# Kernel tuning notes

Measured on AMD Instinct MI355X. Metric: run time of the kernel, lower is better.

The kernel has to match this reference:

```python
import jax, jax.numpy as jnp
import numpy as np

B, L, DM = 2, 1024, 768
DI = 2 * DM            # d_inner = 1536
NS = 16                # d_state
DTR = 48               # dt_rank
SCALE = 15             # scale_bits


def _dsp(x):
    # DampenedSquareplus: 0.5 * squareplus(x) = 0.25*(x + sqrt(x^2+4))
    return 0.25 * (x + jnp.sqrt(x * x + 4.0))


def _forward(hidden_states, gamma, W_in, b_in, conv_w, conv_b, W_x, b_x,
             W_dt, b_dt, W_out, b_out, base_decay_nums, res_gate, decay_shifts):
    residual = hidden_states
    # BitShiftNorm: center, then power-of-two RMS scale
    xm = hidden_states - hidden_states.mean(axis=-1, keepdims=True)
    var = (xm * xm).mean(axis=-1, keepdims=True)
    k = jnp.maximum(jnp.round(jnp.log2(jnp.sqrt(var + 1e-9))), 0.0)
    hs = xm * (2.0 ** (-k)) * gamma
    # in_proj (BitLinear modeled as linear)
    xz = hs @ W_in.T + b_in                      # [B,L,2*DI]
    x, z = jnp.split(xz, 2, axis=-1)             # each [B,L,DI]
    # causal depthwise conv1d (kernel 4, left pad 3, truncate to L)
    xt = jnp.transpose(x, (0, 2, 1))             # [B,DI,L]
    xt = jax.lax.conv_general_dilated(
        xt, conv_w, window_strides=(1,), padding=[(3, 0)],
        dimension_numbers=('NCH', 'OIH', 'NCH'), feature_group_count=DI)
    xt = xt + conv_b[None, :, None]
    x = jnp.transpose(xt, (0, 2, 1))             # [B,L,DI]
    x = _dsp(x)
    # x_proj -> dt, B_ssm, C_ssm
    x_dbl = x @ W_x.T + b_x                      # [B,L,DTR+2*NS]
    dt = x_dbl[..., :DTR]
    B_ssm = x_dbl[..., DTR:DTR + NS]
    C_ssm = x_dbl[..., DTR + NS:]
    decay_mod = dt @ W_dt.T + b_dt               # [B,L,DI]
    decay_nums = jnp.clip(base_decay_nums[None, None] + decay_mod[..., None], 0.0, 32767.0)  # [B,L,DI,NS]
    dt_val = _dsp(decay_mod) * 0.1               # [B,L,DI]
    u = (x * dt_val)[..., None] * B_ssm[:, :, None, :]   # [B,L,DI,NS]
    # dyadic decay: a = nums * 2^{-shift}
    a = decay_nums * (2.0 ** (-decay_shifts.astype(jnp.float32)))[None, None]
    F = DI * NS
    u_f = u.reshape(B, L, F)
    a_f = a.reshape(B, L, F)
    # linear recurrence h_t = a_t*h_{t-1} + u_t via associative scan over L
    def combine(c1, c2):
        a1, b1 = c1
        a2, b2 = c2
        return (a1 * a2, a2 * b1 + b2)
    _, h_f = jax.lax.associative_scan(combine, (a_f, u_f), axis=1)
    h_f = jnp.clip(h_f, -32000.0, 32000.0)
    h = h_f.reshape(B, L, DI, NS)
    y = jnp.einsum('bldn,bln->bld', h, C_ssm)    # [B,L,DI]
    # RationalSigmoid gate
    gate = 0.5 * (1.0 + z / jnp.sqrt(z * z + 1.0))
    y = y * gate
    out = y @ W_out.T + b_out
    out = jnp.clip(out, -32000.0, 32000.0)
    return residual + out * res_gate


def setup_inputs() -> dict:
    key = jax.random.key(0)
    ks = jax.random.split(key, 8)
    hidden_states = jax.random.normal(ks[0], (B, L, DM), jnp.float32)
    gamma = jnp.ones((DM,), jnp.float32)
    W_in = jax.random.normal(ks[1], (2 * DI, DM), jnp.float32) / np.float32(np.sqrt(DM))
    b_in = jnp.zeros((2 * DI,), jnp.float32)
    conv_w = jax.random.normal(ks[2], (DI, 1, 4), jnp.float32) * 0.5
    conv_b = jnp.zeros((DI,), jnp.float32)
    W_x = jax.random.normal(ks[3], (DTR + 2 * NS, DI), jnp.float32) / np.float32(np.sqrt(DI))
    b_x = jnp.zeros((DTR + 2 * NS,), jnp.float32)
    W_dt = jax.random.normal(ks[4], (DI, DTR), jnp.float32) * 0.001
    b_dt = jnp.zeros((DI,), jnp.float32)
    W_out = jax.random.normal(ks[5], (DM, DI), jnp.float32) * np.float32(0.02 / np.sqrt(24))
    b_out = jnp.zeros((DM,), jnp.float32)
    # HiPPO-S4D-real-like decays projected to dyadic with shift=15
    n = jnp.arange(NS, dtype=jnp.float32)
    decays = jnp.exp(-0.01 * (n + 1.0))
    base = jnp.round(decays * (2.0 ** SCALE))
    base_decay_nums = jnp.tile(base[None, :], (DI, 1))
    decay_shifts = jnp.full((DI, NS), SCALE, jnp.int32)
    res_gate = jnp.full((1,), 0.5, jnp.float32)  # nonzero so output depends on branch
    return dict(hidden_states=hidden_states, gamma=gamma, W_in=W_in, b_in=b_in,
                conv_w=conv_w, conv_b=conv_b, W_x=W_x, b_x=b_x, W_dt=W_dt, b_dt=b_dt,
                W_out=W_out, b_out=b_out, base_decay_nums=base_decay_nums,
                res_gate=res_gate, decay_shifts=decay_shifts)


def reference(hidden_states, gamma, W_in, b_in, conv_w, conv_b, W_x, b_x,
              W_dt, b_dt, W_out, b_out, base_decay_nums, res_gate, decay_shifts):
    return _forward(hidden_states, gamma, W_in, b_in, conv_w, conv_b, W_x, b_x,
                    W_dt, b_dt, W_out, b_out, base_decay_nums, res_gate, decay_shifts)
```

## Files before the change

kernel.cpp:

```cpp
#include <hip/hip_runtime.h>
#include <hip/hip_bf16.h>
#include <stdint.h>

#define BB  2
#define LL  1024
#define DMM 768
#define DII 1536
#define NSS 16
#define DTRR 48
#define XZN (2*DII)
#define NROWS (BB*LL)
#define N2 1664

#define CHUNKS 64
#define CHLEN  (LL/CHUNKS)
#define NCH    (BB*DII*NSS)

typedef _Float16 h16;
typedef __attribute__((ext_vector_type(8))) _Float16 h16x8;
typedef __attribute__((ext_vector_type(4))) float f32x4;

typedef const __attribute__((address_space(1))) uint32_t gau32;
typedef __attribute__((address_space(3))) uint32_t lau32;
#define GLL16(gp, lp) __builtin_amdgcn_global_load_lds((gau32*)(gp), (lau32*)(lp), 16, 0, 0)

__device__ __forceinline__ float dspf(float x) {
    return 0.25f * (x + sqrtf(x*x + 4.0f));
}
__device__ __forceinline__ float clampf(float x, float lo, float hi) {
    return fminf(fmaxf(x, lo), hi);
}

#define CVT_BLOCKS ((XZN*DMM + DMM*DII)/256)
#define W2_BLOCKS  N2
#define NORM_BLOCKS (NROWS/4)

__global__ __launch_bounds__(256) void k_prep(
    const float* __restrict__ W_in,  h16* __restrict__ WINH,
    const float* __restrict__ W_out, h16* __restrict__ WOH,
    const float* __restrict__ W_x,   const float* __restrict__ b_x,
    const float* __restrict__ W_dt,  const float* __restrict__ b_dt,
    h16* __restrict__ W2, float* __restrict__ bias2,
    const float* __restrict__ hs, const float* __restrict__ gamma,
    h16* __restrict__ HSNH)
{
    __shared__ float wd[DTRR];
    int blk = blockIdx.x;
    int tid = threadIdx.x;

    if (blk < CVT_BLOCKS) {
        int i = blk * 256 + tid;
        const int n1 = XZN * DMM;
        if (i < n1) WINH[i] = (h16)W_in[i];
        else        WOH[i - n1] = (h16)W_out[i - n1];
        return;
    }
    blk -= CVT_BLOCKS;
    if (blk < W2_BLOCKS) {
        int i = blk;
        if (i < DII) {
            if (tid < DTRR) wd[tid] = W_dt[i * DTRR + tid];
            __syncthreads();
            for (int j = tid; j < DII; j += 256) {
                float s = 0.f;
                #pragma unroll
                for (int k = 0; k < DTRR; ++k) s = fmaf(wd[k], W_x[(size_t)k * DII + j], s);
                W2[(size_t)i * DII + j] = (h16)s;
            }
            if (tid == 0) {
                float s = b_dt[i];
                for (int k = 0; k < DTRR; ++k) s = fmaf(wd[k], b_x[k], s);
                bias2[i] = s;
            }
        } else if (i < DII + 2 * NSS) {
            int r = i - DII;
            for (int j = tid; j < DII; j += 256)
                W2[(size_t)i * DII + j] = (h16)W_x[(size_t)(DTRR + r) * DII + j];
            if (tid == 0) bias2[i] = b_x[DTRR + r];
        } else {
            for (int j = tid; j < DII; j += 256) W2[(size_t)i * DII + j] = (h16)0.f;
            if (tid == 0) bias2[i] = 0.f;
        }
        return;
    }
    blk -= W2_BLOCKS;
    int row  = blk * 4 + (tid >> 6);
    int lane = tid & 63;
    const float* p = hs + (size_t)row * DMM;
    float4 v0 = *(const float4*)&p[lane * 4];
    float4 v1 = *(const float4*)&p[256 + lane * 4];
    float4 v2 = *(const float4*)&p[512 + lane * 4];
    float s = v0.x+v0.y+v0.z+v0.w + v1.x+v1.y+v1.z+v1.w + v2.x+v2.y+v2.z+v2.w;
    #pragma unroll
    for (int off = 32; off > 0; off >>= 1) s += __shfl_xor(s, off);
    float mean = s * (1.0f / (float)DMM);
    float vv = 0.f;
    #pragma unroll
    for (int q = 0; q < 4; ++q) {
        float d0 = ((const float*)&v0)[q] - mean; vv += d0*d0;
        float d1 = ((const float*)&v1)[q] - mean; vv += d1*d1;
        float d2 = ((const float*)&v2)[q] - mean; vv += d2*d2;
    }
    #pragma unroll
    for (int off = 32; off > 0; off >>= 1) vv += __shfl_xor(vv, off);
    float var = vv * (1.0f / (float)DMM);
    float k = rintf(log2f(sqrtf(var + 1e-9f)));
    k = fmaxf(k, 0.f);
    float scale = exp2f(-k);
    float4 g0 = *(const float4*)&gamma[lane * 4];
    float4 g1 = *(const float4*)&gamma[256 + lane * 4];
    float4 g2 = *(const float4*)&gamma[512 + lane * 4];
    h16* o = HSNH + (size_t)row * DMM;
    #pragma unroll
    for (int q = 0; q < 4; ++q) {
        o[lane*4 + q]       = (h16)((((const float*)&v0)[q] - mean) * scale * ((const float*)&g0)[q]);
        o[256 + lane*4 + q] = (h16)((((const float*)&v1)[q] - mean) * scale * ((const float*)&g1)[q]);
        o[512 + lane*4 + q] = (h16)((((const float*)&v2)[q] - mean) * scale * ((const float*)&g2)[q]);
    }
}

template<int EPI, typename OutT>
__global__ __launch_bounds__(256) void k_gemm128(
    const h16* __restrict__ A, int lda,
    const h16* __restrict__ Bw, int ldb,
    const float* __restrict__ bias,
    OutT* __restrict__ C, int ldc, int K,
    const float* __restrict__ resid, const float* __restrict__ rgate)
{
    __shared__ __align__(16) h16 As[2][128 * 64];
    __shared__ __align__(16) h16 Bs[2][128 * 64];
    const int tid  = threadIdx.x;
    const int lane = tid & 63;
    const int wv   = tid >> 6;

    const int nwg = gridDim.x * gridDim.y;
    const int bid = blockIdx.y * gridDim.x + blockIdx.x;
    const int cpx = nwg >> 3;
    const int swz = (bid & 7) * cpx + (bid >> 3);
    const int bxi = swz % gridDim.x, byi = swz / gridDim.x;

    const int bm = byi * 128, bn = bxi * 128;
    const int wr = wv >> 1, wc = wv & 1;

    f32x4 acc[4][4] = {};

    const int srow = lane >> 3;
    const int kbl  = ((lane & 7) ^ srow) * 8;
    const int KT = K / 64;

#define STAGE128(dstbuf, k0) do { \
    _Pragma("unroll") \
    for (int q = 0; q < 4; ++q) { \
        int row_ = (wv * 4 + q) * 8 + srow; \
        GLL16(A  + (size_t)(bm + row_) * lda + (k0) + kbl, &As[dstbuf][(wv*4+q)*8*64]); \
        GLL16(Bw + (size_t)(bn + row_) * ldb + (k0) + kbl, &Bs[dstbuf][(wv*4+q)*8*64]); \
    } } while (0)

    STAGE128(0, 0);
    int buf = 0;
    const int r16 = lane & 15, kq = lane >> 4;

    for (int kt = 0; kt < KT; ++kt) {
        if (kt + 1 < KT) {
            STAGE128(buf ^ 1, (kt + 1) * 64);
            asm volatile("s_waitcnt vmcnt(8)" ::: "memory");
        } else {
            asm volatile("s_waitcnt vmcnt(0)" ::: "memory");
        }
        __syncthreads();
        #pragma unroll
        for (int kk = 0; kk < 2; ++kk) {
            h16x8 af[4], bf[4];
            #pragma unroll
            for (int i = 0; i < 4; ++i) {
                int rowA = wr * 64 + i * 16 + r16;
                af[i] = *(const h16x8*)&As[buf][rowA * 64 + (((kk*4 + kq) ^ (rowA & 7)) << 3)];
            }
            #pragma unroll
            for (int j = 0; j < 4; ++j) {
                int rowB = wc * 64 + j * 16 + r16;
                bf[j] = *(const h16x8*)&Bs[buf][rowB * 64 + (((kk*4 + kq) ^ (rowB & 7)) << 3)];
            }
            #pragma unroll
            for (int i = 0; i < 4; ++i)
                #pragma unroll
                for (int j = 0; j < 4; ++j)
                    acc[i][j] = __builtin_amdgcn_mfma_f32_16x16x32_f16(af[i], bf[j], acc[i][j], 0, 0, 0);
        }
        __syncthreads();
        buf ^= 1;
    }
#undef STAGE128

    const int r4 = (lane >> 4) * 4;
    const int cn = lane & 15;
    float rg = 0.f;
    if (EPI == 1) rg = rgate[0];
    #pragma unroll
    for (int i = 0; i < 4; ++i) {
        #pragma unroll
        for (int j = 0; j < 4; ++j) {
            int col = bn + wc * 64 + j * 16 + cn;
            float bv = bias[col];
            #pragma unroll
            for (int r = 0; r < 4; ++r) {
                int row = bm + wr * 64 + i * 16 + r4 + r;
                float v = acc[i][j][r] + bv;
                if (EPI == 1) {
                    v = clampf(v, -32000.f, 32000.f);
                    v = resid[(size_t)row * ldc + col] + v * rg;
                }
                if (EPI == 2) {
                    if (col >= DII) v = 0.5f * (1.0f + v * rsqrtf(v * v + 1.0f));
                }
                C[(size_t)row * ldc + col] = (OutT)v;
            }
        }
    }
}

template<int EPI, typename OutT>
__global__ __launch_bounds__(256) void k_gemm64(
    const h16* __restrict__ A, int lda,
    const h16* __restrict__ Bw, int ldb,
    const float* __restrict__ bias,
    OutT* __restrict__ C, int ldc, int K,
    const float* __restrict__ resid, const float* __restrict__ rgate)
{
    __shared__ __align__(16) h16 As[2][64 * 64];
    __shared__ __align__(16) h16 Bs[2][64 * 64];
    const int tid  = threadIdx.x;
    const int lane = tid & 63;
    const int wv   = tid >> 6;

    const int nwg = gridDim.x * gridDim.y;
    const int bid = blockIdx.y * gridDim.x + blockIdx.x;
    const int cpx = nwg >> 3;
    const int swz = (bid & 7) * cpx + (bid >> 3);
    const int bxi = swz % gridDim.x, byi = swz / gridDim.x;

    const int bm = byi * 64, bn = bxi * 64;
    const int wr = wv >> 1, wc = wv & 1;

    f32x4 acc[2][2] = {};

    const int srow = lane >> 3;
    const int kbl  = ((lane & 7) ^ srow) * 8;
    const int KT = K / 64;

    #pragma unroll
    for (int q = 0; q < 2; ++q) {
        int row = (wv * 2 + q) * 8 + srow;
        GLL16(A  + (size_t)(bm + row) * lda + kbl, &As[0][(wv*2+q)*8*64]);
        GLL16(Bw + (size_t)(bn + row) * ldb + kbl, &Bs[0][(wv*2+q)*8*64]);
    }

    int buf = 0;
    for (int kt = 0; kt < KT; ++kt) {
        if (kt + 1 < KT) {
            int k0 = (kt + 1) * 64;
            #pragma unroll
            for (int q = 0; q < 2; ++q) {
                int row = (wv * 2 + q) * 8 + srow;
                GLL16(A  + (size_t)(bm + row) * lda + k0 + kbl, &As[buf^1][(wv*2+q)*8*64]);
                GLL16(Bw + (size_t)(bn + row) * ldb + k0 + kbl, &Bs[buf^1][(wv*2+q)*8*64]);
            }
            asm volatile("s_waitcnt vmcnt(4)" ::: "memory");
        } else {
            asm volatile("s_waitcnt vmcnt(0)" ::: "memory");
        }
        __syncthreads();

        const int r16 = lane & 15, kq = lane >> 4;
        #pragma unroll
        for (int kk = 0; kk < 2; ++kk) {
            h16x8 af[2], bf[2];
            #pragma unroll
            for (int i = 0; i < 2; ++i) {
                int rowA = wr * 32 + i * 16 + r16;
                af[i] = *(const h16x8*)&As[buf][rowA * 64 + (((kk*4 + kq) ^ (rowA & 7)) << 3)];
            }
            #pragma unroll
            for (int j = 0; j < 2; ++j) {
                int rowB = wc * 32 + j * 16 + r16;
                bf[j] = *(const h16x8*)&Bs[buf][rowB * 64 + (((kk*4 + kq) ^ (rowB & 7)) << 3)];
            }
            #pragma unroll
            for (int i = 0; i < 2; ++i)
                #pragma unroll
                for (int j = 0; j < 2; ++j)
                    acc[i][j] = __builtin_amdgcn_mfma_f32_16x16x32_f16(af[i], bf[j], acc[i][j], 0, 0, 0);
        }
        __syncthreads();
        buf ^= 1;
    }

    const int r4 = (lane >> 4) * 4;
    const int cn = lane & 15;
    float rg = 0.f;
    if (EPI == 1) rg = rgate[0];
    #pragma unroll
    for (int i = 0; i < 2; ++i) {
        #pragma unroll
        for (int j = 0; j < 2; ++j) {
            int col = bn + wc * 32 + j * 16 + cn;
            float bv = bias[col];
            #pragma unroll
            for (int r = 0; r < 4; ++r) {
                int row = bm + wr * 32 + i * 16 + r4 + r;
                float v = acc[i][j][r] + bv;
                if (EPI == 1) {
                    v = clampf(v, -32000.f, 32000.f);
                    v = resid[(size_t)row * ldc + col] + v * rg;
                }
                C[(size_t)row * ldc + col] = (OutT)v;
            }
        }
    }
}

__global__ __launch_bounds__(256) void k_conv(const h16* __restrict__ xz,
                                              const float* __restrict__ cw,
                                              const float* __restrict__ cb,
                                              h16* __restrict__ xacth)
{
    int idx = blockIdx.x * 256 + threadIdx.x;
    if (idx >= NROWS * (DII / 8)) return;
    int c8 = idx % (DII / 8);
    int bl = idx / (DII / 8);
    int l = bl % LL;
    int b = bl / LL;
    int c0 = c8 * 8;

    float acc[8];
    float4 wv[8];
    #pragma unroll
    for (int j = 0; j < 8; ++j) {
        acc[j] = cb[c0 + j];
        wv[j] = *(const float4*)&cw[(c0 + j) * 4];
    }
    #pragma unroll
    for (int t = 0; t < 4; ++t) {
        int ls = l - 3 + t;
        if (ls >= 0) {
            h16x8 xv = *(const h16x8*)&xz[(size_t)(b * LL + ls) * XZN + c0];
            #pragma unroll
            for (int j = 0; j < 8; ++j)
                acc[j] = fmaf((float)xv[j], ((const float*)&wv[j])[t], acc[j]);
        }
    }
    h16x8 o;
    #pragma unroll
    for (int j = 0; j < 8; ++j) o[j] = (h16)dspf(acc[j]);
    *(h16x8*)&xacth[(size_t)bl * DII + c0] = o;
}

__device__ __forceinline__ void load_setup(const float* __restrict__ basenum,
                                           const int* __restrict__ shifts,
                                           int d, float* baseP, float* p2c) {
    const float4* bp = (const float4*)(basenum + (size_t)d * NSS);
    const int4*   sp = (const int4*)(shifts + (size_t)d * NSS);
    #pragma unroll
    for (int q = 0; q < 4; ++q) {
        float4 bv = bp[q]; int4 sv = sp[q];
        p2c[q*4+0] = exp2f(-(float)sv.x);
        p2c[q*4+1] = exp2f(-(float)sv.y);
        p2c[q*4+2] = exp2f(-(float)sv.z);
        p2c[q*4+3] = exp2f(-(float)sv.w);
        baseP[q*4+0] = bv.x * p2c[q*4+0];
        baseP[q*4+1] = bv.y * p2c[q*4+1];
        baseP[q*4+2] = bv.z * p2c[q*4+2];
        baseP[q*4+3] = bv.w * p2c[q*4+3];
    }
}

__global__ __launch_bounds__(256) void k_scan_p1(
    const h16* __restrict__ dmbc,
    const h16* __restrict__ xacth,
    const float* __restrict__ basenum,
    const int*   __restrict__ shifts,
    float* __restrict__ stA, float* __restrict__ stH)
{
    int bc   = blockIdx.x / 6;
    int dblk = blockIdx.x % 6;
    int d    = dblk * 256 + threadIdx.x;
    int b    = bc / CHUNKS;
    int chunk= bc % CHUNKS;

    float baseP[16], p2c[16], h[16], A[16];
    load_setup(basenum, shifts, d, baseP, p2c);
    #pragma unroll
    for (int n = 0; n < 16; ++n) { h[n] = 0.f; A[n] = 1.f; }

    int row0 = b * LL + chunk * CHLEN;
    #pragma unroll 4
    for (int l = 0; l < CHLEN; ++l) {
        int row = row0 + l;
        float dm = (float)dmbc[(size_t)row * N2 + d];
        float xv = (float)xacth[(size_t)row * DII + d];
        float common = xv * (dspf(dm) * 0.1f);
        const h16x8* Bp = (const h16x8*)(dmbc + (size_t)row * N2 + DII);
        h16x8 b0 = Bp[0], b1 = Bp[1];
        float Bv[16];
        #pragma unroll
        for (int n = 0; n < 8; ++n) { Bv[n] = (float)b0[n]; Bv[8+n] = (float)b1[n]; }
        #pragma unroll
        for (int n = 0; n < 16; ++n) {
            float a = fmaf(dm, p2c[n], baseP[n]);
            h[n] = fmaf(a, h[n], common * Bv[n]);
            A[n] *= a;
        }
    }
    size_t sb = ((size_t)bc * DII + d) * 16;
    float4* pa = (float4*)(stA + sb);
    float4* ph = (float4*)(stH + sb);
    #pragma unroll
    for (int q = 0; q < 4; ++q) {
        pa[q] = make_float4(A[q*4+0], A[q*4+1], A[q*4+2], A[q*4+3]);
        ph[q] = make_float4(h[q*4+0], h[q*4+1], h[q*4+2], h[q*4+3]);
    }
}

__global__ __launch_bounds__(256) void k_scan_p2(float* __restrict__ stA,
                                                 const float* __restrict__ stH)
{
    int ch = blockIdx.x * 256 + threadIdx.x;
    int b  = ch / (DII * NSS);
    int rem = ch - b * (DII * NSS);
    float hin = 0.f;
    #pragma unroll 4
    for (int c = 0; c < CHUNKS; ++c) {
        size_t idx = ((size_t)(b * CHUNKS + c) * (DII * NSS)) + rem;
        float a = stA[idx], hh = stH[idx];
        stA[idx] = hin;
        hin = fmaf(a, hin, hh);
    }
}

__global__ __launch_bounds__(256) void k_scan_p3(
    const h16* __restrict__ dmbc,
    const h16* __restrict__ xacth,
    const h16* __restrict__ xz,
    const float* __restrict__ basenum,
    const int*   __restrict__ shifts,
    const float* __restrict__ stA,
    h16* __restrict__ ygh)
{
    int bc   = blockIdx.x / 6;
    int dblk = blockIdx.x % 6;
    int d    = dblk * 256 + threadIdx.x;
    int b    = bc / CHUNKS;
    int chunk= bc % CHUNKS;

    float baseP[16], p2c[16], h[16];
    load_setup(basenum, shifts, d, baseP, p2c);
    size_t sb = ((size_t)bc * DII + d) * 16;
    const float4* pa = (const float4*)(stA + sb);
    #pragma unroll
    for (int q = 0; q < 4; ++q) {
        float4 v = pa[q];
        h[q*4+0] = v.x; h[q*4+1] = v.y; h[q*4+2] = v.z; h[q*4+3] = v.w;
    }

    int row0 = b * LL + chunk * CHLEN;
    #pragma unroll 4
    for (int l = 0; l < CHLEN; ++l) {
        int row = row0 + l;
        float dm = (float)dmbc[(size_t)row * N2 + d];
        float xv = (float)xacth[(size_t)row * DII + d];
        float common = xv * (dspf(dm) * 0.1f);
        const h16x8* Bp = (const h16x8*)(dmbc + (size_t)row * N2 + DII);
        h16x8 b0 = Bp[0], b1 = Bp[1], c0 = Bp[2], c1 = Bp[3];
        float Bv[16], Cv[16];
        #pragma unroll
        for (int n = 0; n < 8; ++n) {
            Bv[n] = (float)b0[n]; Bv[8+n] = (float)b1[n];
            Cv[n] = (float)c0[n]; Cv[8+n] = (float)c1[n];
        }
        float y = 0.f;
        #pragma unroll
        for (int n = 0; n < 16; ++n) {
            float a = fmaf(dm, p2c[n], baseP[n]);
            h[n] = fmaf(a, h[n], common * Bv[n]);
            float hc = clampf(h[n], -32000.f, 32000.f);
            y = fmaf(hc, Cv[n], y);
        }
        float gate = (float)xz[(size_t)row * XZN + DII + d];
        ygh[(size_t)row * DII + d] = (h16)(y * gate);
    }
}

extern "C" void kernel_launch(void* const* d_in, const int* in_sizes, int n_in,
                              void* d_out, int out_size, void* d_ws, size_t ws_size,
                              hipStream_t stream) {
    const float* hs        = (const float*)d_in[0];
    const float* gamma     = (const float*)d_in[1];
    const float* W_in      = (const float*)d_in[2];
    const float* b_in      = (const float*)d_in[3];
    const float* conv_w    = (const float*)d_in[4];
    const float* conv_b    = (const float*)d_in[5];
    const float* W_x       = (const float*)d_in[6];
    const float* b_x       = (const float*)d_in[7];
    const float* W_dt      = (const float*)d_in[8];
    const float* b_dt      = (const float*)d_in[9];
    const float* W_out     = (const float*)d_in[10];
    const float* b_out     = (const float*)d_in[11];
    const float* base_dec  = (const float*)d_in[12];
    const float* res_gate  = (const float*)d_in[13];
    const int*   dec_shift = (const int*)d_in[14];

    char* w = (char*)d_ws;
    h16*   XZH   = (h16*)w;    w += (size_t)NROWS * XZN * 2;
    h16*   XACTH = (h16*)w;    w += (size_t)NROWS * DII * 2;
    h16*   DMBCH = (h16*)w;    w += (size_t)NROWS * N2  * 2;
    h16*   W2H   = (h16*)w;    w += (size_t)N2 * DII * 2;
    h16*   WOH   = (h16*)w;    w += (size_t)DMM * DII * 2;
    float* BIAS2 = (float*)w;  w += 8192;
    h16*   YGH   = (h16*)w;    w += (size_t)NROWS * DII * 2;
    h16*   HSNH  = (h16*)w;    w += (size_t)NROWS * DMM * 2;
    h16*   WINH  = (h16*)w;    w += (size_t)XZN * DMM * 2;
    float* STA   = (float*)w;  w += (size_t)BB * CHUNKS * DII * NSS * 4;
    float* STH   = (float*)w;  w += (size_t)BB * CHUNKS * DII * NSS * 4;

    float* out = (float*)d_out;

    k_prep<<<CVT_BLOCKS + W2_BLOCKS + NORM_BLOCKS, 256, 0, stream>>>(
        W_in, WINH, W_out, WOH, W_x, b_x, W_dt, b_dt, W2H, BIAS2,
        hs, gamma, HSNH);

    k_gemm128<2, h16><<<dim3(XZN / 128, NROWS / 128), 256, 0, stream>>>(
        HSNH, DMM, WINH, DMM, b_in, XZH, XZN, DMM, nullptr, nullptr);

    k_conv<<<(NROWS * (DII / 8)) / 256, 256, 0, stream>>>(XZH, conv_w, conv_b, XACTH);

    k_gemm128<0, h16><<<dim3(N2 / 128, NROWS / 128), 256, 0, stream>>>(
        XACTH, DII, W2H, DII, BIAS2, DMBCH, N2, DII, nullptr, nullptr);

    k_scan_p1<<<BB * CHUNKS * 6, 256, 0, stream>>>(
        DMBCH, XACTH, base_dec, dec_shift, STA, STH);
    k_scan_p2<<<NCH / 256, 256, 0, stream>>>(STA, STH);
    k_scan_p3<<<BB * CHUNKS * 6, 256, 0, stream>>>(
        DMBCH, XACTH, XZH, base_dec, dec_shift, STA, YGH);

    k_gemm64<1, float><<<dim3(DMM / 64, NROWS / 64), 256, 0, stream>>>(
        YGH, DII, WOH, DII, b_out, out, DMM, DII, hs, res_gate);
}
```

Before: 168.3 us.

## Split scan state dimension across half-waves and shrink p2 blocks

```diff
diff --git a/kernel.cpp b/kernel.cpp
--- a/kernel.cpp
+++ b/kernel.cpp
@@ -355,13 +355,14 @@
     *(h16x8*)&xacth[(size_t)bl * DII + c0] = o;
 }
 
-__device__ __forceinline__ void load_setup(const float* __restrict__ basenum,
-                                           const int* __restrict__ shifts,
-                                           int d, float* baseP, float* p2c) {
-    const float4* bp = (const float4*)(basenum + (size_t)d * NSS);
-    const int4*   sp = (const int4*)(shifts + (size_t)d * NSS);
-    #pragma unroll
-    for (int q = 0; q < 4; ++q) {
+__device__ __forceinline__ void load_setup8(const float* __restrict__ basenum,
+                                            const int* __restrict__ shifts,
+                                            int d, int nbase,
+                                            float* baseP, float* p2c) {
+    const float4* bp = (const float4*)(basenum + (size_t)d * NSS + nbase);
+    const int4*   sp = (const int4*)(shifts  + (size_t)d * NSS + nbase);
+    #pragma unroll
+    for (int q = 0; q < 2; ++q) {
         float4 bv = bp[q]; int4 sv = sp[q];
         p2c[q*4+0] = exp2f(-(float)sv.x);
         p2c[q*4+1] = exp2f(-(float)sv.y);
@@ -381,16 +382,20 @@
     const int*   __restrict__ shifts,
     float* __restrict__ stA, float* __restrict__ stH)
 {
-    int bc   = blockIdx.x / 6;
-    int dblk = blockIdx.x % 6;
-    int d    = dblk * 256 + threadIdx.x;
+    int bc   = blockIdx.x / 12;
+    int dblk = blockIdx.x % 12;
+    int tid  = threadIdx.x;
+    int lane = tid & 63, wv = tid >> 6;
+    int half = lane >> 5;
+    int d    = dblk * 128 + wv * 32 + (lane & 31);
     int b    = bc / CHUNKS;
     int chunk= bc % CHUNKS;
-
-    float baseP[16], p2c[16], h[16], A[16];
-    load_setup(basenum, shifts, d, baseP, p2c);
-    #pragma unroll
-    for (int n = 0; n < 16; ++n) { h[n] = 0.f; A[n] = 1.f; }
+    int nbase = half * 8;
+
+    float baseP[8], p2c[8], h[8], A[8];
+    load_setup8(basenum, shifts, d, nbase, baseP, p2c);
+    #pragma unroll
+    for (int n = 0; n < 8; ++n) { h[n] = 0.f; A[n] = 1.f; }
 
     int row0 = b * LL + chunk * CHLEN;
     #pragma unroll 4
@@ -399,32 +404,27 @@
         float dm = (float)dmbc[(size_t)row * N2 + d];
         float xv = (float)xacth[(size_t)row * DII + d];
         float common = xv * (dspf(dm) * 0.1f);
-        const h16x8* Bp = (const h16x8*)(dmbc + (size_t)row * N2 + DII);
-        h16x8 b0 = Bp[0], b1 = Bp[1];
-        float Bv[16];
+        h16x8 bv8 = *(const h16x8*)&dmbc[(size_t)row * N2 + DII + nbase];
         #pragma unroll
-        for (int n = 0; n < 8; ++n) { Bv[n] = (float)b0[n]; Bv[8+n] = (float)b1[n]; }
-        #pragma unroll
-        for (int n = 0; n < 16; ++n) {
+        for (int n = 0; n < 8; ++n) {
             float a = fmaf(dm, p2c[n], baseP[n]);
-            h[n] = fmaf(a, h[n], common * Bv[n]);
+            h[n] = fmaf(a, h[n], common * (float)bv8[n]);
             A[n] *= a;
         }
     }
-    size_t sb = ((size_t)bc * DII + d) * 16;
+    size_t sb = ((size_t)bc * DII + d) * 16 + nbase;
     float4* pa = (float4*)(stA + sb);
     float4* ph = (float4*)(stH + sb);
-    #pragma unroll
-    for (int q = 0; q < 4; ++q) {
-        pa[q] = make_float4(A[q*4+0], A[q*4+1], A[q*4+2], A[q*4+3]);
-        ph[q] = make_float4(h[q*4+0], h[q*4+1], h[q*4+2], h[q*4+3]);
-    }
-}
-
-__global__ __launch_bounds__(256) void k_scan_p2(float* __restrict__ stA,
-                                                 const float* __restrict__ stH)
-{
-    int ch = blockIdx.x * 256 + threadIdx.x;
+    pa[0] = make_float4(A[0], A[1], A[2], A[3]);
+    pa[1] = make_float4(A[4], A[5], A[6], A[7]);
+    ph[0] = make_float4(h[0], h[1], h[2], h[3]);
+    ph[1] = make_float4(h[4], h[5], h[6], h[7]);
+}
+
+__global__ __launch_bounds__(64) void k_scan_p2(float* __restrict__ stA,
+                                                const float* __restrict__ stH)
+{
+    int ch = blockIdx.x * 64 + threadIdx.x;
     int b  = ch / (DII * NSS);
     int rem = ch - b * (DII * NSS);
     float hin = 0.f;
@@ -446,20 +446,24 @@
     const float* __restrict__ stA,
     h16* __restrict__ ygh)
 {
-    int bc   = blockIdx.x / 6;
-    int dblk = blockIdx.x % 6;
-    int d    = dblk * 256 + threadIdx.x;
+    int bc   = blockIdx.x / 12;
+    int dblk = blockIdx.x % 12;
+    int tid  = threadIdx.x;
+    int lane = tid & 63, wv = tid >> 6;
+    int half = lane >> 5;
+    int d    = dblk * 128 + wv * 32 + (lane & 31);
     int b    = bc / CHUNKS;
     int chunk= bc % CHUNKS;
-
-    float baseP[16], p2c[16], h[16];
-    load_setup(basenum, shifts, d, baseP, p2c);
-    size_t sb = ((size_t)bc * DII + d) * 16;
-    const float4* pa = (const float4*)(stA + sb);
-    #pragma unroll
-    for (int q = 0; q < 4; ++q) {
-        float4 v = pa[q];
-        h[q*4+0] = v.x; h[q*4+1] = v.y; h[q*4+2] = v.z; h[q*4+3] = v.w;
+    int nbase = half * 8;
+
+    float baseP[8], p2c[8], h[8];
+    load_setup8(basenum, shifts, d, nbase, baseP, p2c);
+    size_t sb = ((size_t)bc * DII + d) * 16 + nbase;
+    {
+        const float4* pa = (const float4*)(stA + sb);
+        float4 v0 = pa[0], v1 = pa[1];
+        h[0]=v0.x; h[1]=v0.y; h[2]=v0.z; h[3]=v0.w;
+        h[4]=v1.x; h[5]=v1.y; h[6]=v1.z; h[7]=v1.w;
     }
 
     int row0 = b * LL + chunk * CHLEN;
@@ -469,24 +473,21 @@
         float dm = (float)dmbc[(size_t)row * N2 + d];
         float xv = (float)xacth[(size_t)row * DII + d];
         float common = xv * (dspf(dm) * 0.1f);
-        const h16x8* Bp = (const h16x8*)(dmbc + (size_t)row * N2 + DII);
-        h16x8 b0 = Bp[0], b1 = Bp[1], c0 = Bp[2], c1 = Bp[3];
-        float Bv[16], Cv[16];
+        h16x8 bv8 = *(const h16x8*)&dmbc[(size_t)row * N2 + DII + nbase];
+        h16x8 cv8 = *(const h16x8*)&dmbc[(size_t)row * N2 + DII + NSS + nbase];
+        float y = 0.f;
         #pragma unroll
         for (int n = 0; n < 8; ++n) {
-            Bv[n] = (float)b0[n]; Bv[8+n] = (float)b1[n];
-            Cv[n] = (float)c0[n]; Cv[8+n] = (float)c1[n];
-        }
-        float y = 0.f;
-        #pragma unroll
-        for (int n = 0; n < 16; ++n) {
             float a = fmaf(dm, p2c[n], baseP[n]);
-            h[n] = fmaf(a, h[n], common * Bv[n]);
+            h[n] = fmaf(a, h[n], common * (float)bv8[n]);
             float hc = clampf(h[n], -32000.f, 32000.f);
-            y = fmaf(hc, Cv[n], y);
-        }
-        float gate = (float)xz[(size_t)row * XZN + DII + d];
-        ygh[(size_t)row * DII + d] = (h16)(y * gate);
+            y = fmaf(hc, (float)cv8[n], y);
+        }
+        y += __shfl_xor(y, 32);
+        if (half == 0) {
+            float gate = (float)xz[(size_t)row * XZN + DII + d];
+            ygh[(size_t)row * DII + d] = (h16)(y * gate);
+        }
     }
 }
 
@@ -536,10 +537,10 @@
     k_gemm128<0, h16><<<dim3(N2 / 128, NROWS / 128), 256, 0, stream>>>(
         XACTH, DII, W2H, DII, BIAS2, DMBCH, N2, DII, nullptr, nullptr);
 
-    k_scan_p1<<<BB * CHUNKS * 6, 256, 0, stream>>>(
+    k_scan_p1<<<BB * CHUNKS * 12, 256, 0, stream>>>(
         DMBCH, XACTH, base_dec, dec_shift, STA, STH);
-    k_scan_p2<<<NCH / 256, 256, 0, stream>>>(STA, STH);
-    k_scan_p3<<<BB * CHUNKS * 6, 256, 0, stream>>>(
+    k_scan_p2<<<NCH / 64, 64, 0, stream>>>(STA, STH);
+    k_scan_p3<<<BB * CHUNKS * 12, 256, 0, stream>>>(
         DMBCH, XACTH, XZH, base_dec, dec_shift, STA, YGH);
 
     k_gemm64<1, float><<<dim3(DMM / 64, NROWS / 64), 256, 0, stream>>>(
```

Measured after the change: 171.0 us. Within noise of the previous version (+1.6%).
